# Optimization experiments

Measured on AMD Instinct MI355X. Metric: run time of the kernel, lower is better.

Reference implementation:

```python
import jax, jax.numpy as jnp
import numpy as np

B, S, D_IN, D_OUT = 4, 2048, 1024, 1024


def setup_inputs() -> dict:
    key = jax.random.key(0)
    ks = jax.random.split(key, 6)
    scale = 1.0 / np.sqrt(D_IN)
    return {
        "inputs_for_keys": jax.random.normal(ks[0], (B, S, D_IN), jnp.float32),
        "inputs_for_values": jax.random.normal(ks[1], (B, S, D_IN), jnp.float32),
        "inputs_for_queries": jax.random.normal(ks[2], (B, S, D_IN), jnp.float32),
        "WK": jax.random.uniform(ks[3], (D_IN, D_OUT), jnp.float32, -scale, scale),
        "WQ": jax.random.uniform(ks[4], (D_IN, D_OUT), jnp.float32, -scale, scale),
        "WV": jax.random.uniform(ks[5], (D_IN, D_OUT), jnp.float32, -scale, scale),
    }


def reference(inputs_for_keys, inputs_for_values, inputs_for_queries, WK, WQ, WV):
    # QKV projections: [B,S,Din] @ [Din,Dout] -> [B,S,Dout]
    keys = jnp.einsum("bsd,de->bse", inputs_for_keys, WK)
    values = jnp.einsum("bsd,de->bse", inputs_for_values, WV)
    queries = jnp.einsum("bsd,de->bse", inputs_for_queries, WQ)
    d_k = keys.shape[-1]
    # scaled scores [B,S,S]
    scores = jnp.einsum("bqe,bke->bqk", queries, keys) / jnp.sqrt(jnp.float32(d_k))
    # causal mask: position k > q gets -inf (strictly upper triangular)
    q_idx = jnp.arange(S)[:, None]
    k_idx = jnp.arange(S)[None, :]
    scores = jnp.where(k_idx > q_idx, -jnp.inf, scores)
    att = jax.nn.softmax(scores, axis=-1)
    out = jnp.einsum("bqk,bke->bqe", att, values)  # [B,S,Dout]
    return out
```

## Files before the change

### kernel.cpp

```cpp
#include <hip/hip_runtime.h>
#include <stdint.h>


typedef __attribute__((ext_vector_type(8))) short short8;
typedef __attribute__((ext_vector_type(8))) unsigned short ushort8;
typedef __attribute__((ext_vector_type(4))) float f32x4;

__device__ __forceinline__ unsigned short f2bf(float f) {
  union { float f; unsigned u; } v; v.f = f;
  unsigned u = v.u + 0x7FFFu + ((v.u >> 16) & 1u);
  return (unsigned short)(u >> 16);
}
__device__ __forceinline__ float bf2f(unsigned short h) {
  union { unsigned u; float f; } v; v.u = ((unsigned)h) << 16;
  return v.f;
}

__device__ __forceinline__ void gload16(const void* g, void* l) {
  __builtin_amdgcn_global_load_lds(
      (const __attribute__((address_space(1))) unsigned int*)g,
      (__attribute__((address_space(3))) unsigned int*)l, 16, 0, 0);
}

template<int N> __device__ __forceinline__ void vmwait() {
  static_assert(N >= 0 && N <= 8, "vmcnt range");
  if constexpr (N == 0) asm volatile("s_waitcnt vmcnt(0)" ::: "memory");
  else if constexpr (N == 1) asm volatile("s_waitcnt vmcnt(1)" ::: "memory");
  else if constexpr (N == 2) asm volatile("s_waitcnt vmcnt(2)" ::: "memory");
  else if constexpr (N == 3) asm volatile("s_waitcnt vmcnt(3)" ::: "memory");
  else if constexpr (N == 4) asm volatile("s_waitcnt vmcnt(4)" ::: "memory");
  else if constexpr (N == 5) asm volatile("s_waitcnt vmcnt(5)" ::: "memory");
  else if constexpr (N == 6) asm volatile("s_waitcnt vmcnt(6)" ::: "memory");
  else if constexpr (N == 7) asm volatile("s_waitcnt vmcnt(7)" ::: "memory");
  else asm volatile("s_waitcnt vmcnt(8)" ::: "memory");
}
__device__ __forceinline__ void barrier_() { asm volatile("s_barrier" ::: "memory"); }
__device__ __forceinline__ void lgkm0() { asm volatile("s_waitcnt lgkmcnt(0)" ::: "memory"); }

__global__ __launch_bounds__(256)
void prep(const float* __restrict__ Xq, const float* __restrict__ Xk,
          const float* __restrict__ Xv,
          unsigned short* __restrict__ Oq, unsigned short* __restrict__ Ok,
          unsigned short* __restrict__ Ov,
          const float* __restrict__ WQ, const float* __restrict__ WK,
          const float* __restrict__ WV,
          unsigned short* __restrict__ WQT, unsigned short* __restrict__ WKT,
          unsigned short* __restrict__ WVT) {
  const int bx = blockIdx.x;
  const int tid = threadIdx.x;
  if (bx < 12288) {
    const int op = bx >> 12, r = bx & 4095;
    const float* in = op == 0 ? Xq : op == 1 ? Xk : Xv;
    unsigned short* out = op == 0 ? Oq : op == 1 ? Ok : Ov;
    const long i = ((long)r * 256 + tid) * 8;
    float4 a = *(const float4*)(in + i);
    float4 b = *(const float4*)(in + i + 4);
    ushort8 rr;
    rr[0] = f2bf(a.x); rr[1] = f2bf(a.y); rr[2] = f2bf(a.z); rr[3] = f2bf(a.w);
    rr[4] = f2bf(b.x); rr[5] = f2bf(b.y); rr[6] = f2bf(b.z); rr[7] = f2bf(b.w);
    *(ushort8*)(out + i) = rr;
  } else {
    const int t = bx - 12288;
    const int z = t >> 10, rem = t & 1023;
    const float* W = z == 0 ? WQ : z == 1 ? WK : WV;
    unsigned short* WT = z == 0 ? WQT : z == 1 ? WKT : WVT;
    const float scale = z == 0 ? 0.03125f : 1.0f;
    __shared__ float tbuf[32][33];
    const int bk = (rem >> 5) * 32, be = (rem & 31) * 32;
    const int tx = tid & 31, ty = tid >> 5;
#pragma unroll
    for (int j = 0; j < 32; j += 8)
      tbuf[ty + j][tx] = W[(long)(bk + ty + j) * 1024 + (be + tx)];
    __syncthreads();
#pragma unroll
    for (int j = 0; j < 32; j += 8)
      WT[(long)(be + ty + j) * 1024 + (bk + tx)] = f2bf(tbuf[tx][ty + j] * scale);
  }
}

template<typename CT, int MF, int NF>
__device__ __forceinline__ void gemm_body(const unsigned short* __restrict__ A,
                                          const unsigned short* __restrict__ B,
                                          CT* __restrict__ C,
                                          int bm, int bn, int kmax,
                                          int lda, int ldb, int ldc,
                                          char* AL, char* BL) {
  constexpr int BM = MF * 32, BN = NF * 64;
  constexpr int LA = BM / 128, LB = BN / 128;
  constexpr int S = 2 * (LA + LB);

  const int tid = threadIdx.x;
  const int lane = tid & 63, wid = tid >> 6;
  const int wr = wid >> 2, wc = wid & 3;
  const int fr = lane & 15, fq = lane >> 4;
  const int srow = tid >> 2;
  const int scol = (((tid & 3) ^ ((tid >> 3) & 3)) << 3);
  const int m0 = bm * BM, n0 = bn * BN;
  const int nt = kmax >> 6;

  f32x4 acc[MF][NF] = {};

  const unsigned short* As = A + (long)(m0 + srow) * lda + scol;
  const unsigned short* Bs = B + (long)(n0 + srow) * ldb + scol;

  auto stageTile = [&](int b, int kt) {
#pragma unroll
    for (int h = 0; h < 2; ++h) {
#pragma unroll
      for (int l = 0; l < LA; ++l)
        gload16(As + (long)l * 128 * lda + kt * 64 + h * 32,
                AL + b * (BM * 128) + h * (BM * 64) + l * 8192 + tid * 16);
#pragma unroll
      for (int l = 0; l < LB; ++l)
        gload16(Bs + (long)l * 128 * ldb + kt * 64 + h * 32,
                BL + b * (BN * 128) + h * (BN * 64) + l * 8192 + tid * 16);
    }
  };

  const int aoff = (wr * (BM / 2) + fr) * 64 + ((fq ^ ((fr >> 1) & 3)) << 4);
  const int boff = (wc * (BN / 4) + fr) * 64 + ((fq ^ ((fr >> 1) & 3)) << 4);
  auto ardf = [&](int b, int kk, int m) -> short8 {
    return *(const short8*)(AL + b * (BM * 128) + kk * (BM * 64) + aoff + m * 1024);
  };
  auto brdf = [&](int b, int kk, int n) -> short8 {
    return *(const short8*)(BL + b * (BN * 128) + kk * (BN * 64) + boff + n * 1024);
  };

  stageTile(0, 0);

  for (int u = 0; u < nt; ++u) {
    const int cb = u & 1, nb = cb ^ 1;
    lgkm0();
    barrier_();
    if (u + 1 < nt) { stageTile(nb, u + 1); vmwait<S>(); }
    else            { vmwait<0>(); }
    barrier_();
#pragma unroll
    for (int kk = 0; kk < 2; ++kk) {
      short8 bfr[NF], af[MF / 2];
#pragma unroll
      for (int n = 0; n < NF; ++n) bfr[n] = brdf(cb, kk, n);
#pragma unroll
      for (int m = 0; m < MF / 2; ++m) af[m] = ardf(cb, kk, m);
      __builtin_amdgcn_s_setprio(1);
#pragma unroll
      for (int m = 0; m < MF / 2; ++m)
#pragma unroll
        for (int n = 0; n < NF; ++n)
          acc[m][n] = __builtin_amdgcn_mfma_f32_16x16x32_bf16(af[m], bfr[n], acc[m][n], 0, 0, 0);
      __builtin_amdgcn_s_setprio(0);
#pragma unroll
      for (int m = 0; m < MF / 2; ++m) af[m] = ardf(cb, kk, MF / 2 + m);
      __builtin_amdgcn_s_setprio(1);
#pragma unroll
      for (int m = 0; m < MF / 2; ++m)
#pragma unroll
        for (int n = 0; n < NF; ++n)
          acc[MF / 2 + m][n] =
              __builtin_amdgcn_mfma_f32_16x16x32_bf16(af[m], bfr[n], acc[MF / 2 + m][n], 0, 0, 0);
      __builtin_amdgcn_s_setprio(0);
    }
  }

#pragma unroll
  for (int m = 0; m < MF; ++m) {
    const int row = m0 + wr * (BM / 2) + m * 16 + fq * 4;
#pragma unroll
    for (int n = 0; n < NF; ++n) {
      const int col = n0 + wc * (BN / 4) + n * 16 + fr;
#pragma unroll
      for (int r = 0; r < 4; ++r) {
        float v = acc[m][n][r];
        if constexpr (sizeof(CT) == 2)
          C[(long)(row + r) * ldc + col] = (CT)f2bf(v);
        else
          C[(long)(row + r) * ldc + col] = (CT)v;
      }
    }
  }
}

__global__ __launch_bounds__(512, 2)
void qkvt_gemm(const unsigned short* __restrict__ Xq, const unsigned short* __restrict__ WQT,
               unsigned short* __restrict__ Q,
               const unsigned short* __restrict__ Xk, const unsigned short* __restrict__ WKT,
               unsigned short* __restrict__ Kk,
               const unsigned short* __restrict__ WVT, const unsigned short* __restrict__ Xv,
               unsigned short* __restrict__ VT) {
  __shared__ __align__(16) char pool[131072];
  const int id = (blockIdx.x & 7) * 32 + (blockIdx.x >> 3);
  if (id < 128)
    gemm_body<unsigned short, 8, 4>(Xq, WQT, Q, id >> 2, id & 3, 1024,
                                    1024, 1024, 1024, pool, pool + 65536);
  else
    gemm_body<unsigned short, 8, 4>(Xk, WKT, Kk, (id - 128) >> 2, id & 3, 1024,
                                    1024, 1024, 1024, pool, pool + 65536);
  __syncthreads();
  gemm_body<unsigned short, 4, 4>(WVT, Xv, VT, id >> 5, id & 31, 1024,
                                  1024, 1024, 8192, pool, pool + 32768);
}

__global__ __launch_bounds__(512, 4)
void scores_gemm(const unsigned short* __restrict__ Q, const unsigned short* __restrict__ K,
                 unsigned short* __restrict__ S) {
  __shared__ __align__(16) char pool[65536];
  const int gid = (blockIdx.x & 7) * 68 + (blockIdx.x >> 3);
  const int bz = gid / 136, t = gid - bz * 136;
  int bm = (int)((__fsqrt_rn(8.0f * t + 1.0f) - 1.0f) * 0.5f);
  while ((bm + 1) * (bm + 2) / 2 <= t) ++bm;
  while (bm * (bm + 1) / 2 > t) --bm;
  const int bn = t - bm * (bm + 1) / 2;
  gemm_body<unsigned short, 4, 2>(Q + (long)bz * 2048 * 1024, K + (long)bz * 2048 * 1024,
                                  S + (long)bz * 2048 * 2048, bm, bn, 1024,
                                  1024, 1024, 2048, pool, pool + 32768);
}

__global__ __launch_bounds__(512, 4)
void pv_gemm(const unsigned short* __restrict__ P, const unsigned short* __restrict__ VT,
             float* __restrict__ O) {
  __shared__ __align__(16) char pool[65536];
  const int b = blockIdx.x;
  int bm, r;
  if (b < 256) { bm = 15 - (b >> 5); r = b & 31; }
  else         { bm = (b - 256) >> 5; r = b & 31; }
  const int bn = r & 7, bz = r >> 3;
  gemm_body<float, 4, 2>(P + (long)bz * 2048 * 2048, VT + (long)bz * 2048,
                         O + (long)bz * 2048 * 1024, bm, bn, (bm + 1) * 128,
                         2048, 8192, 1024, pool, pool + 32768);
}

__global__ __launch_bounds__(256)
void softmax_causal(unsigned short* __restrict__ P) {
  const int row = blockIdx.x;
  const int q = row & 2047;
  unsigned short* p = P + (long)row * 2048;
  const int nfill = ((q >> 7) + 1) << 7;
  const int tid = threadIdx.x;
  const int lane = tid & 63, wid = tid >> 6;
  const int i0 = tid * 8;
  __shared__ float red[8];

  float v[8];
  float lmax = -3.0e38f;
  if (i0 <= q) {
    ushort8 v8 = *(const ushort8*)(p + i0);
#pragma unroll
    for (int j = 0; j < 8; ++j) {
      float f = bf2f(v8[j]);
      f = (i0 + j <= q) ? f : -3.0e38f;
      v[j] = f;
      lmax = fmaxf(lmax, f);
    }
  } else {
#pragma unroll
    for (int j = 0; j < 8; ++j) v[j] = -3.0e38f;
  }
#pragma unroll
  for (int off = 1; off < 64; off <<= 1)
    lmax = fmaxf(lmax, __shfl_xor(lmax, off));
  if (lane == 0) red[wid] = lmax;
  __syncthreads();
  const float mx = fmaxf(fmaxf(red[0], red[1]), fmaxf(red[2], red[3]));

  float lsum = 0.f;
#pragma unroll
  for (int j = 0; j < 8; ++j) {
    float e = __expf(v[j] - mx);
    v[j] = e;
    lsum += e;
  }
#pragma unroll
  for (int off = 1; off < 64; off <<= 1)
    lsum += __shfl_xor(lsum, off);
  if (lane == 0) red[4 + wid] = lsum;
  __syncthreads();
  const float inv = 1.0f / (red[4] + red[5] + red[6] + red[7]);

  if (i0 < nfill) {
    ushort8 r;
#pragma unroll
    for (int j = 0; j < 8; ++j)
      r[j] = (i0 + j <= q) ? f2bf(v[j] * inv) : (unsigned short)0;
    *(ushort8*)(p + i0) = r;
  }
}

extern "C" void kernel_launch(void* const* d_in, const int* in_sizes, int n_in,
                              void* d_out, int out_size, void* d_ws, size_t ws_size,
                              hipStream_t stream) {
  const float* Xk = (const float*)d_in[0];
  const float* Xv = (const float*)d_in[1];
  const float* Xq = (const float*)d_in[2];
  const float* WK = (const float*)d_in[3];
  const float* WQ = (const float*)d_in[4];
  const float* WV = (const float*)d_in[5];
  float* out = (float*)d_out;

  unsigned short* ws = (unsigned short*)d_ws;
  const long NE = 8L * 1024 * 1024;
  unsigned short* Xqb = ws + 0 * NE;
  unsigned short* Xkb = ws + 1 * NE;
  unsigned short* Xvb = ws + 2 * NE;
  unsigned short* Qb  = ws + 3 * NE;
  unsigned short* Kb  = ws + 4 * NE;
  unsigned short* VTb = ws + 5 * NE;
  unsigned short* WQT = ws + 6 * NE;
  unsigned short* WKT = WQT + 1024 * 1024;
  unsigned short* WVT = WKT + 1024 * 1024;
  unsigned short* Sc  = ws;

  dim3 b256(256), b512(512);
  prep<<<15360, b256, 0, stream>>>(Xq, Xk, Xv, Xqb, Xkb, Xvb,
                                   WQ, WK, WV, WQT, WKT, WVT);
  qkvt_gemm<<<256, b512, 0, stream>>>(Xqb, WQT, Qb, Xkb, WKT, Kb, WVT, Xvb, VTb);
  scores_gemm<<<544, b512, 0, stream>>>(Qb, Kb, Sc);
  softmax_causal<<<8192, b256, 0, stream>>>(Sc);
  pv_gemm<<<512, b512, 0, stream>>>(Sc, VTb, out);
}
```

Measured before the change: 163.0 us.

## Use four-phase interleaved load/MFMA pipeline for QKV projection GEMMs

Adds a new GEMM body that splits each 64-wide K tile into four phases. Each phase interleaves LDS fragment reads, prefetch of the next tile's half-slices, and a half of the MFMA work, with barriers and s_setprio raising priority around the MFMA blocks. The QKV projection kernel now uses it in place of the generic gemm_body. The aim is to overlap global-to-LDS loads with matrix math and smooth issue contention, at the cost of more barriers per tile.

```diff
diff --git a/kernel.cpp b/kernel.cpp
--- a/kernel.cpp
+++ b/kernel.cpp
@@ -78,6 +78,7 @@
   }
 }
 
+
 template<typename CT, int MF, int NF>
 __device__ __forceinline__ void gemm_body(const unsigned short* __restrict__ A,
                                           const unsigned short* __restrict__ B,
@@ -180,6 +181,129 @@
   }
 }
 
+template<int MF, int NF>
+__device__ __forceinline__ void gemm_4ph(const unsigned short* __restrict__ A,
+                                         const unsigned short* __restrict__ B,
+                                         unsigned short* __restrict__ C,
+                                         int bm, int bn, int kmax,
+                                         int lda, int ldb, int ldc,
+                                         char* AL, char* BL) {
+  constexpr int BM = MF * 32, BN = NF * 64;
+  constexpr int LA = BM / 128, LB = BN / 128;
+
+  const int tid = threadIdx.x;
+  const int lane = tid & 63, wid = tid >> 6;
+  const int wr = wid >> 2, wc = wid & 3;
+  const int fr = lane & 15, fq = lane >> 4;
+  const int srow = tid >> 2;
+  const int scol = (((tid & 3) ^ ((tid >> 3) & 3)) << 3);
+  const int m0 = bm * BM, n0 = bn * BN;
+  const int nt = kmax >> 6;
+
+  f32x4 acc[MF][NF] = {};
+
+  const unsigned short* As = A + (long)(m0 + srow) * lda + scol;
+  const unsigned short* Bs = B + (long)(n0 + srow) * ldb + scol;
+
+  auto stageA = [&](int b, int h, int kt) {
+#pragma unroll
+    for (int l = 0; l < LA; ++l)
+      gload16(As + (long)l * 128 * lda + kt * 64 + h * 32,
+              AL + b * (BM * 128) + h * (BM * 64) + l * 8192 + tid * 16);
+  };
+  auto stageB = [&](int b, int h, int kt) {
+#pragma unroll
+    for (int l = 0; l < LB; ++l)
+      gload16(Bs + (long)l * 128 * ldb + kt * 64 + h * 32,
+              BL + b * (BN * 128) + h * (BN * 64) + l * 8192 + tid * 16);
+  };
+
+  const int aoff = (wr * (BM / 2) + fr) * 64 + ((fq ^ ((fr >> 1) & 3)) << 4);
+  const int boff = (wc * (BN / 4) + fr) * 64 + ((fq ^ ((fr >> 1) & 3)) << 4);
+  auto ardf = [&](int b, int kk, int m) -> short8 {
+    return *(const short8*)(AL + b * (BM * 128) + kk * (BM * 64) + aoff + m * 1024);
+  };
+  auto brdf = [&](int b, int kk, int n) -> short8 {
+    return *(const short8*)(BL + b * (BN * 128) + kk * (BN * 64) + boff + n * 1024);
+  };
+
+  stageA(0, 0, 0); stageB(0, 0, 0); stageA(0, 1, 0); stageB(0, 1, 0);
+
+  short8 bfr[NF], af[MF / 2];
+  for (int u = 0; u < nt; ++u) {
+    const int cb = u & 1, nb = cb ^ 1;
+    const bool pf = (u + 1 < nt);
+    if (pf) { stageA(nb, 0, u + 1); vmwait<LA>(); }
+    else    { vmwait<0>(); }
+    barrier_();
+#pragma unroll
+    for (int n = 0; n < NF; ++n) bfr[n] = brdf(cb, 0, n);
+#pragma unroll
+    for (int m = 0; m < MF / 2; ++m) af[m] = ardf(cb, 0, m);
+    if (pf) stageB(nb, 0, u + 1);
+    barrier_();
+    __builtin_amdgcn_s_setprio(1);
+#pragma unroll
+    for (int m = 0; m < MF / 2; ++m)
+#pragma unroll
+      for (int n = 0; n < NF; ++n)
+        acc[m][n] = __builtin_amdgcn_mfma_f32_16x16x32_bf16(af[m], bfr[n], acc[m][n], 0, 0, 0);
+    __builtin_amdgcn_s_setprio(0);
+    barrier_();
+#pragma unroll
+    for (int m = 0; m < MF / 2; ++m) af[m] = ardf(cb, 0, MF / 2 + m);
+    if (pf) stageA(nb, 1, u + 1);
+    barrier_();
+    __builtin_amdgcn_s_setprio(1);
+#pragma unroll
+    for (int m = 0; m < MF / 2; ++m)
+#pragma unroll
+      for (int n = 0; n < NF; ++n)
+        acc[MF / 2 + m][n] =
+            __builtin_amdgcn_mfma_f32_16x16x32_bf16(af[m], bfr[n], acc[MF / 2 + m][n], 0, 0, 0);
+    __builtin_amdgcn_s_setprio(0);
+    barrier_();
+#pragma unroll
+    for (int n = 0; n < NF; ++n) bfr[n] = brdf(cb, 1, n);
+#pragma unroll
+    for (int m = 0; m < MF / 2; ++m) af[m] = ardf(cb, 1, m);
+    if (pf) stageB(nb, 1, u + 1);
+    barrier_();
+    __builtin_amdgcn_s_setprio(1);
+#pragma unroll
+    for (int m = 0; m < MF / 2; ++m)
+#pragma unroll
+      for (int n = 0; n < NF; ++n)
+        acc[m][n] = __builtin_amdgcn_mfma_f32_16x16x32_bf16(af[m], bfr[n], acc[m][n], 0, 0, 0);
+    __builtin_amdgcn_s_setprio(0);
+    barrier_();
+#pragma unroll
+    for (int m = 0; m < MF / 2; ++m) af[m] = ardf(cb, 1, MF / 2 + m);
+    barrier_();
+    __builtin_amdgcn_s_setprio(1);
+#pragma unroll
+    for (int m = 0; m < MF / 2; ++m)
+#pragma unroll
+      for (int n = 0; n < NF; ++n)
+        acc[MF / 2 + m][n] =
+            __builtin_amdgcn_mfma_f32_16x16x32_bf16(af[m], bfr[n], acc[MF / 2 + m][n], 0, 0, 0);
+    __builtin_amdgcn_s_setprio(0);
+    barrier_();
+  }
+
+#pragma unroll
+  for (int m = 0; m < MF; ++m) {
+    const int row = m0 + wr * (BM / 2) + m * 16 + fq * 4;
+#pragma unroll
+    for (int n = 0; n < NF; ++n) {
+      const int col = n0 + wc * (BN / 4) + n * 16 + fr;
+#pragma unroll
+      for (int r = 0; r < 4; ++r)
+        C[(long)(row + r) * ldc + col] = f2bf(acc[m][n][r]);
+    }
+  }
+}
+
 __global__ __launch_bounds__(512, 2)
 void qkvt_gemm(const unsigned short* __restrict__ Xq, const unsigned short* __restrict__ WQT,
                unsigned short* __restrict__ Q,
@@ -190,14 +314,14 @@
   __shared__ __align__(16) char pool[131072];
   const int id = (blockIdx.x & 7) * 32 + (blockIdx.x >> 3);
   if (id < 128)
-    gemm_body<unsigned short, 8, 4>(Xq, WQT, Q, id >> 2, id & 3, 1024,
-                                    1024, 1024, 1024, pool, pool + 65536);
+    gemm_4ph<8, 4>(Xq, WQT, Q, id >> 2, id & 3, 1024,
+                   1024, 1024, 1024, pool, pool + 65536);
   else
-    gemm_body<unsigned short, 8, 4>(Xk, WKT, Kk, (id - 128) >> 2, id & 3, 1024,
-                                    1024, 1024, 1024, pool, pool + 65536);
+    gemm_4ph<8, 4>(Xk, WKT, Kk, (id - 128) >> 2, id & 3, 1024,
+                   1024, 1024, 1024, pool, pool + 65536);
   __syncthreads();
-  gemm_body<unsigned short, 4, 4>(WVT, Xv, VT, id >> 5, id & 31, 1024,
-                                  1024, 1024, 8192, pool, pool + 32768);
+  gemm_4ph<4, 4>(WVT, Xv, VT, id >> 5, id & 31, 1024,
+                 1024, 1024, 8192, pool, pool + 32768);
 }
 
 __global__ __launch_bounds__(512, 4)
```

Result: faster. 158.2 us (-3.0%).

## Reassociate QK^T as Xq·(WQ·WK^T)·Xk^T to skip the K projection

Applied to the files above, without the earlier changes.

The product WQ·WK^T (1024x1024) is precomputed, with the 1/sqrt(d) scale folded into WQ. Xq is multiplied by it to get Y, and scores are computed directly against bf16 Xk, so the full K projection GEMM disappears. The V projection and the small M GEMM share one launch, followed by a separate Y GEMM. Weight prep for WQ/WK becomes a plain convert instead of a transpose, and the score buffer now aliases the dead Xq/Xv bf16 buffers. The cost is an extra kernel launch and an additional bf16 rounding of the combined weight matrix.

```diff
diff --git a/kernel.cpp b/kernel.cpp
--- a/kernel.cpp
+++ b/kernel.cpp
@@ -44,7 +44,7 @@
           unsigned short* __restrict__ Ov,
           const float* __restrict__ WQ, const float* __restrict__ WK,
           const float* __restrict__ WV,
-          unsigned short* __restrict__ WQT, unsigned short* __restrict__ WKT,
+          unsigned short* __restrict__ WQb, unsigned short* __restrict__ WKb,
           unsigned short* __restrict__ WVT) {
   const int bx = blockIdx.x;
   const int tid = threadIdx.x;
@@ -59,22 +59,32 @@
     rr[0] = f2bf(a.x); rr[1] = f2bf(a.y); rr[2] = f2bf(a.z); rr[3] = f2bf(a.w);
     rr[4] = f2bf(b.x); rr[5] = f2bf(b.y); rr[6] = f2bf(b.z); rr[7] = f2bf(b.w);
     *(ushort8*)(out + i) = rr;
+  } else if (bx < 13312) {
+    const int wi = bx - 12288;
+    const float* in = wi < 512 ? WQ : WK;
+    unsigned short* out = wi < 512 ? WQb : WKb;
+    const float scale = wi < 512 ? 0.03125f : 1.0f;
+    const long i = ((long)(wi & 511) * 256 + tid) * 8;
+    float4 a = *(const float4*)(in + i);
+    float4 b = *(const float4*)(in + i + 4);
+    ushort8 rr;
+    rr[0] = f2bf(a.x * scale); rr[1] = f2bf(a.y * scale);
+    rr[2] = f2bf(a.z * scale); rr[3] = f2bf(a.w * scale);
+    rr[4] = f2bf(b.x * scale); rr[5] = f2bf(b.y * scale);
+    rr[6] = f2bf(b.z * scale); rr[7] = f2bf(b.w * scale);
+    *(ushort8*)(out + i) = rr;
   } else {
-    const int t = bx - 12288;
-    const int z = t >> 10, rem = t & 1023;
-    const float* W = z == 0 ? WQ : z == 1 ? WK : WV;
-    unsigned short* WT = z == 0 ? WQT : z == 1 ? WKT : WVT;
-    const float scale = z == 0 ? 0.03125f : 1.0f;
+    const int rem = bx - 13312;
     __shared__ float tbuf[32][33];
     const int bk = (rem >> 5) * 32, be = (rem & 31) * 32;
     const int tx = tid & 31, ty = tid >> 5;
 #pragma unroll
     for (int j = 0; j < 32; j += 8)
-      tbuf[ty + j][tx] = W[(long)(bk + ty + j) * 1024 + (be + tx)];
+      tbuf[ty + j][tx] = WV[(long)(bk + ty + j) * 1024 + (be + tx)];
     __syncthreads();
 #pragma unroll
     for (int j = 0; j < 32; j += 8)
-      WT[(long)(be + ty + j) * 1024 + (bk + tx)] = f2bf(tbuf[tx][ty + j] * scale);
+      WVT[(long)(be + ty + j) * 1024 + (bk + tx)] = f2bf(tbuf[tx][ty + j]);
   }
 }
 
@@ -180,28 +190,34 @@
   }
 }
 
-__global__ __launch_bounds__(512, 2)
-void qkvt_gemm(const unsigned short* __restrict__ Xq, const unsigned short* __restrict__ WQT,
-               unsigned short* __restrict__ Q,
-               const unsigned short* __restrict__ Xk, const unsigned short* __restrict__ WKT,
-               unsigned short* __restrict__ Kk,
-               const unsigned short* __restrict__ WVT, const unsigned short* __restrict__ Xv,
-               unsigned short* __restrict__ VT) {
-  __shared__ __align__(16) char pool[131072];
-  const int id = (blockIdx.x & 7) * 32 + (blockIdx.x >> 3);
-  if (id < 128)
-    gemm_body<unsigned short, 8, 4>(Xq, WQT, Q, id >> 2, id & 3, 1024,
-                                    1024, 1024, 1024, pool, pool + 65536);
-  else
-    gemm_body<unsigned short, 8, 4>(Xk, WKT, Kk, (id - 128) >> 2, id & 3, 1024,
-                                    1024, 1024, 1024, pool, pool + 65536);
-  __syncthreads();
-  gemm_body<unsigned short, 4, 4>(WVT, Xv, VT, id >> 5, id & 31, 1024,
-                                  1024, 1024, 8192, pool, pool + 32768);
-}
-
 __global__ __launch_bounds__(512, 4)
-void scores_gemm(const unsigned short* __restrict__ Q, const unsigned short* __restrict__ K,
+void d2_gemm(const unsigned short* __restrict__ WVT, const unsigned short* __restrict__ Xvb,
+             unsigned short* __restrict__ VT,
+             const unsigned short* __restrict__ WKb, const unsigned short* __restrict__ WQb,
+             unsigned short* __restrict__ Mt) {
+  __shared__ __align__(16) char pool[65536];
+  const int id = (blockIdx.x & 7) * 72 + (blockIdx.x >> 3);
+  if (id < 512)
+    gemm_body<unsigned short, 4, 2>(WVT, Xvb, VT, id >> 6, id & 63, 1024,
+                                    1024, 1024, 8192, pool, pool + 32768);
+  else {
+    const int t = id - 512;
+    gemm_body<unsigned short, 4, 2>(WKb, WQb, Mt, t >> 3, t & 7, 1024,
+                                    1024, 1024, 1024, pool, pool + 32768);
+  }
+}
+
+__global__ __launch_bounds__(512, 4)
+void y_gemm(const unsigned short* __restrict__ Xqb, const unsigned short* __restrict__ Mt,
+            unsigned short* __restrict__ Y) {
+  __shared__ __align__(16) char pool[65536];
+  const int id = (blockIdx.x & 7) * 64 + (blockIdx.x >> 3);
+  gemm_body<unsigned short, 4, 2>(Xqb, Mt, Y, id >> 3, id & 7, 1024,
+                                  1024, 1024, 1024, pool, pool + 32768);
+}
+
+__global__ __launch_bounds__(512, 4)
+void scores_gemm(const unsigned short* __restrict__ Y, const unsigned short* __restrict__ Xkb,
                  unsigned short* __restrict__ S) {
   __shared__ __align__(16) char pool[65536];
   const int gid = (blockIdx.x & 7) * 68 + (blockIdx.x >> 3);
@@ -210,7 +226,7 @@
   while ((bm + 1) * (bm + 2) / 2 <= t) ++bm;
   while (bm * (bm + 1) / 2 > t) --bm;
   const int bn = t - bm * (bm + 1) / 2;
-  gemm_body<unsigned short, 4, 2>(Q + (long)bz * 2048 * 1024, K + (long)bz * 2048 * 1024,
+  gemm_body<unsigned short, 4, 2>(Y + (long)bz * 2048 * 1024, Xkb + (long)bz * 2048 * 1024,
                                   S + (long)bz * 2048 * 2048, bm, bn, 1024,
                                   1024, 1024, 2048, pool, pool + 32768);
 }
@@ -298,22 +314,23 @@
 
   unsigned short* ws = (unsigned short*)d_ws;
   const long NE = 8L * 1024 * 1024;
-  unsigned short* Xqb = ws + 0 * NE;
-  unsigned short* Xkb = ws + 1 * NE;
+  unsigned short* Xkb = ws + 0 * NE;
+  unsigned short* Xqb = ws + 1 * NE;
   unsigned short* Xvb = ws + 2 * NE;
-  unsigned short* Qb  = ws + 3 * NE;
-  unsigned short* Kb  = ws + 4 * NE;
-  unsigned short* VTb = ws + 5 * NE;
-  unsigned short* WQT = ws + 6 * NE;
-  unsigned short* WKT = WQT + 1024 * 1024;
-  unsigned short* WVT = WKT + 1024 * 1024;
-  unsigned short* Sc  = ws;
+  unsigned short* Yb  = ws + 3 * NE;
+  unsigned short* VTb = ws + 4 * NE;
+  unsigned short* WQb = ws + 5 * NE;
+  unsigned short* WKb = WQb + 1024 * 1024;
+  unsigned short* WVT = WKb + 1024 * 1024;
+  unsigned short* Mtb = WVT + 1024 * 1024;
+  unsigned short* Sc  = ws + 1 * NE;
 
   dim3 b256(256), b512(512);
-  prep<<<15360, b256, 0, stream>>>(Xq, Xk, Xv, Xqb, Xkb, Xvb,
-                                   WQ, WK, WV, WQT, WKT, WVT);
-  qkvt_gemm<<<256, b512, 0, stream>>>(Xqb, WQT, Qb, Xkb, WKT, Kb, WVT, Xvb, VTb);
-  scores_gemm<<<544, b512, 0, stream>>>(Qb, Kb, Sc);
+  prep<<<14336, b256, 0, stream>>>(Xq, Xk, Xv, Xqb, Xkb, Xvb,
+                                   WQ, WK, WV, WQb, WKb, WVT);
+  d2_gemm<<<576, b512, 0, stream>>>(WVT, Xvb, VTb, WKb, WQb, Mtb);
+  y_gemm<<<512, b512, 0, stream>>>(Xqb, Mtb, Yb);
+  scores_gemm<<<544, b512, 0, stream>>>(Yb, Xkb, Sc);
   softmax_causal<<<8192, b256, 0, stream>>>(Sc);
   pv_gemm<<<512, b512, 0, stream>>>(Sc, VTb, out);
 }
```

After: 147.6 us. 1.1x faster.
